# Kernel tuning notes

Hardware: AMD Instinct MI355X
Metric: run time of the kernel (lower is better)

## Reference

```python
import jax, jax.numpy as jnp
import numpy as np

D_MODEL = 768
NHEAD = 12
D_K = D_MODEL // NHEAD


def setup_inputs() -> dict:
    key = jax.random.key(0)
    ks = jax.random.split(key, 9)
    s = 1.0 / np.sqrt(D_MODEL)
    x = jax.random.normal(ks[0], (2, 4096, D_MODEL), dtype=jnp.float32)
    Wq = jax.random.uniform(ks[1], (D_MODEL, D_MODEL), jnp.float32, -s, s)
    bq = jax.random.uniform(ks[2], (D_MODEL,), jnp.float32, -s, s)
    Wk = jax.random.uniform(ks[3], (D_MODEL, D_MODEL), jnp.float32, -s, s)
    bk = jax.random.uniform(ks[4], (D_MODEL,), jnp.float32, -s, s)
    Wv = jax.random.uniform(ks[5], (D_MODEL, D_MODEL), jnp.float32, -s, s)
    bv = jax.random.uniform(ks[6], (D_MODEL,), jnp.float32, -s, s)
    Wo = jax.random.uniform(ks[7], (D_MODEL, D_MODEL), jnp.float32, -s, s)
    bo = jax.random.uniform(ks[8], (D_MODEL,), jnp.float32, -s, s)
    return {"x": x, "Wq": Wq, "bq": bq, "Wk": Wk, "bk": bk,
            "Wv": Wv, "bv": bv, "Wo": Wo, "bo": bo}


def reference(x, Wq, bq, Wk, bk, Wv, bv, Wo, bo):
    B, S, _ = x.shape
    # Linear layers: torch nn.Linear(y) = y @ W.T + b; weights stored [out,in]
    def split_heads(y):  # [B,S,D] -> [B,H,S,dk]
        return y.reshape(B, S, NHEAD, D_K).transpose(0, 2, 1, 3)
    Q = split_heads(x @ Wq.T + bq)
    K = split_heads(x @ Wk.T + bk)
    V = split_heads(x @ Wv.T + bv)
    scores = jnp.einsum('bhqd,bhkd->bhqk', Q, K) / jnp.sqrt(jnp.float32(D_K))
    attn = jax.nn.softmax(scores, axis=-1)
    context = jnp.einsum('bhqk,bhkd->bhqd', attn, V)
    context = context.transpose(0, 2, 1, 3).reshape(B, S, D_MODEL)
    return context @ Wo.T + bo
```

## Files before the change

kernel.cpp:

```cpp
#include <hip/hip_runtime.h>
#include <hip/hip_bf16.h>
#include <cstdint>

typedef __bf16 bf16;
typedef bf16 bf16x8 __attribute__((ext_vector_type(8)));
typedef float f32x4 __attribute__((ext_vector_type(4)));

#define MFMA16(a, b, c) __builtin_amdgcn_mfma_f32_16x16x32_bf16((a), (b), (c), 0, 0, 0)

constexpr int D_MODEL = 768;
constexpr int NHEAD = 12;
constexpr int DK = 64;
constexpr int SEQ = 4096;
constexpr int BATCH = 2;
constexpr int MROWS = BATCH * SEQ;
constexpr float QSCALE = 0.125f * 1.44269504089f;

__global__ void cvt_f32_to_bf16(const float* __restrict__ in, bf16* __restrict__ out, int n) {
    int i = (blockIdx.x * blockDim.x + threadIdx.x) * 4;
    if (i + 3 < n) {
        const float4 v = *reinterpret_cast<const float4*>(in + i);
        bf16 o0 = (bf16)v.x, o1 = (bf16)v.y, o2 = (bf16)v.z, o3 = (bf16)v.w;
        bf16 o[4] = {o0, o1, o2, o3};
        *reinterpret_cast<uint64_t*>(out + i) = *reinterpret_cast<uint64_t*>(o);
    }
}

__global__ __launch_bounds__(256, 2) void gemm_qkv(const bf16* __restrict__ A,
                                                   const float* __restrict__ Wq,
                                                   const float* __restrict__ Wk,
                                                   const float* __restrict__ Wv,
                                                   const float* __restrict__ bq,
                                                   const float* __restrict__ bk,
                                                   const float* __restrict__ bv,
                                                   bf16* __restrict__ Qb,
                                                   bf16* __restrict__ Kb,
                                                   bf16* __restrict__ Vtb) {
    constexpr int LDP = 88;
    __shared__ bf16 Asm[128][LDP];
    __shared__ bf16 Bsm[64][LDP];
    const int tid = threadIdx.x, lane = tid & 63, wid = tid >> 6;
    const int wm = wid >> 1, wn = wid & 1;
    const int m0 = blockIdx.x * 128;
    const int sel = blockIdx.y / 12;
    const int n0 = (blockIdx.y % 12) * 64;
    const float* Bw = sel == 0 ? Wq : (sel == 1 ? Wk : Wv);
    const float* bias = sel == 0 ? bq : (sel == 1 ? bk : bv);

    f32x4 acc[4][2];
#pragma unroll
    for (int i = 0; i < 4; i++)
#pragma unroll
        for (int j = 0; j < 2; j++) acc[i][j] = f32x4{0.f, 0.f, 0.f, 0.f};

    const int rr = tid >> 3, cc = (tid & 7) * 8;
    for (int k0 = 0; k0 < 768; k0 += 64) {
#pragma unroll
        for (int p = 0; p < 4; p++)
            *reinterpret_cast<bf16x8*>(&Asm[p * 32 + rr][cc]) =
                *reinterpret_cast<const bf16x8*>(A + (size_t)(m0 + p * 32 + rr) * 768 + k0 + cc);
#pragma unroll
        for (int p = 0; p < 2; p++) {
            const float* src = Bw + (size_t)(n0 + p * 32 + rr) * 768 + k0 + cc;
            const float4 f0 = *reinterpret_cast<const float4*>(src);
            const float4 f1 = *reinterpret_cast<const float4*>(src + 4);
            bf16x8 b8;
            b8[0] = (bf16)f0.x; b8[1] = (bf16)f0.y; b8[2] = (bf16)f0.z; b8[3] = (bf16)f0.w;
            b8[4] = (bf16)f1.x; b8[5] = (bf16)f1.y; b8[6] = (bf16)f1.z; b8[7] = (bf16)f1.w;
            *reinterpret_cast<bf16x8*>(&Bsm[p * 32 + rr][cc]) = b8;
        }
        __syncthreads();
#pragma unroll
        for (int kk = 0; kk < 64; kk += 32) {
            const int krd = kk + ((lane >> 4) << 3);
            bf16x8 af[4], bfr[2];
#pragma unroll
            for (int i = 0; i < 4; i++)
                af[i] = *reinterpret_cast<const bf16x8*>(&Asm[wm * 64 + i * 16 + (lane & 15)][krd]);
#pragma unroll
            for (int j = 0; j < 2; j++)
                bfr[j] = *reinterpret_cast<const bf16x8*>(&Bsm[wn * 32 + j * 16 + (lane & 15)][krd]);
#pragma unroll
            for (int i = 0; i < 4; i++)
#pragma unroll
                for (int j = 0; j < 2; j++) acc[i][j] = MFMA16(af[i], bfr[j], acc[i][j]);
        }
        __syncthreads();
    }

    const float scale = (sel == 0) ? QSCALE : 1.0f;
    const int rbase = m0 + wm * 64 + ((lane >> 4) << 2);
    const int cbase = n0 + wn * 32 + (lane & 15);
    bf16* obf = sel == 0 ? Qb : (sel == 1 ? Kb : Vtb);
#pragma unroll
    for (int i = 0; i < 4; i++) {
#pragma unroll
        for (int j = 0; j < 2; j++) {
            const int ncol = cbase + j * 16;
            const float bv = bias[ncol];
            const int h = ncol >> 6, d = ncol & 63;
#pragma unroll
            for (int r = 0; r < 4; r++) {
                const int mrow = rbase + i * 16 + r;
                const float v = (acc[i][j][r] + bv) * scale;
                const int b = mrow >> 12, s = mrow & 4095;
                if (sel < 2) {
                    obf[(((size_t)(b * NHEAD + h)) * SEQ + s) * DK + d] = (bf16)v;
                } else {
                    const int sp = (s & ~63) | (((s & 15) << 2) | ((s >> 4) & 3));
                    obf[(((size_t)(b * NHEAD + h)) * DK + d) * SEQ + sp] = (bf16)v;
                }
            }
        }
    }
}

__global__ __launch_bounds__(256, 2) void gemm_out(const bf16* __restrict__ A,
                                                   const float* __restrict__ Bw,
                                                   const float* __restrict__ bias,
                                                   float* __restrict__ ofl) {
    constexpr int LDP = 88;
    __shared__ bf16 Asm[128][LDP];
    __shared__ bf16 Bsm[64][LDP];
    const int tid = threadIdx.x, lane = tid & 63, wid = tid >> 6;
    const int wm = wid >> 1, wn = wid & 1;
    const int m0 = blockIdx.x * 128, n0 = blockIdx.y * 64;

    f32x4 acc[4][2];
#pragma unroll
    for (int i = 0; i < 4; i++)
#pragma unroll
        for (int j = 0; j < 2; j++) acc[i][j] = f32x4{0.f, 0.f, 0.f, 0.f};

    const int rr = tid >> 3, cc = (tid & 7) * 8;
    for (int k0 = 0; k0 < 768; k0 += 64) {
#pragma unroll
        for (int p = 0; p < 4; p++)
            *reinterpret_cast<bf16x8*>(&Asm[p * 32 + rr][cc]) =
                *reinterpret_cast<const bf16x8*>(A + (size_t)(m0 + p * 32 + rr) * 768 + k0 + cc);
#pragma unroll
        for (int p = 0; p < 2; p++) {
            const float* src = Bw + (size_t)(n0 + p * 32 + rr) * 768 + k0 + cc;
            const float4 f0 = *reinterpret_cast<const float4*>(src);
            const float4 f1 = *reinterpret_cast<const float4*>(src + 4);
            bf16x8 b8;
            b8[0] = (bf16)f0.x; b8[1] = (bf16)f0.y; b8[2] = (bf16)f0.z; b8[3] = (bf16)f0.w;
            b8[4] = (bf16)f1.x; b8[5] = (bf16)f1.y; b8[6] = (bf16)f1.z; b8[7] = (bf16)f1.w;
            *reinterpret_cast<bf16x8*>(&Bsm[p * 32 + rr][cc]) = b8;
        }
        __syncthreads();
#pragma unroll
        for (int kk = 0; kk < 64; kk += 32) {
            const int krd = kk + ((lane >> 4) << 3);
            bf16x8 af[4], bfr[2];
#pragma unroll
            for (int i = 0; i < 4; i++)
                af[i] = *reinterpret_cast<const bf16x8*>(&Asm[wm * 64 + i * 16 + (lane & 15)][krd]);
#pragma unroll
            for (int j = 0; j < 2; j++)
                bfr[j] = *reinterpret_cast<const bf16x8*>(&Bsm[wn * 32 + j * 16 + (lane & 15)][krd]);
#pragma unroll
            for (int i = 0; i < 4; i++)
#pragma unroll
                for (int j = 0; j < 2; j++) acc[i][j] = MFMA16(af[i], bfr[j], acc[i][j]);
        }
        __syncthreads();
    }

    const int rbase = m0 + wm * 64 + ((lane >> 4) << 2);
    const int cbase = n0 + wn * 32 + (lane & 15);
#pragma unroll
    for (int i = 0; i < 4; i++) {
#pragma unroll
        for (int j = 0; j < 2; j++) {
            const int ncol = cbase + j * 16;
            const float bv = bias[ncol];
#pragma unroll
            for (int r = 0; r < 4; r++) {
                const int mrow = rbase + i * 16 + r;
                ofl[(size_t)mrow * 768 + ncol] = acc[i][j][r] + bv;
            }
        }
    }
}

__global__ __launch_bounds__(256, 3) void attn_kernel(const bf16* __restrict__ Qb,
                                                      const bf16* __restrict__ Kb,
                                                      const bf16* __restrict__ Vtb,
                                                      bf16* __restrict__ ctx) {
    __shared__ bf16 Ksm[64][72];
    __shared__ bf16 Vts[64][72];
    __shared__ bf16 Psm[4][32][72];
    const int tid = threadIdx.x, l = tid & 63, w = tid >> 6;
    const int bh = blockIdx.y;
    const int q0 = blockIdx.x * 128;
    const bf16* Qh = Qb + (size_t)bh * SEQ * DK;
    const bf16* Kh = Kb + (size_t)bh * SEQ * DK;
    const bf16* Vth = Vtb + (size_t)bh * DK * SEQ;

    const int rsel = l & 15, csel = l >> 4;

    bf16x8 qf[2][2];
#pragma unroll
    for (int qi = 0; qi < 2; qi++) {
        const int qr = q0 + w * 32 + qi * 16 + rsel;
#pragma unroll
        for (int kk = 0; kk < 2; kk++)
            qf[qi][kk] = *reinterpret_cast<const bf16x8*>(Qh + (size_t)qr * DK + kk * 32 + csel * 8);
    }

    bf16x8 vones;
    {
        const bf16 ov = (rsel == 0) ? (bf16)1.0f : (bf16)0.0f;
#pragma unroll
        for (int j = 0; j < 8; j++) vones[j] = ov;
    }

    float m[2] = {-1e30f, -1e30f};
    f32x4 aco[2][4], aco_x[2];
#pragma unroll
    for (int qi = 0; qi < 2; qi++) {
#pragma unroll
        for (int f = 0; f < 4; f++) aco[qi][f] = f32x4{0.f, 0.f, 0.f, 0.f};
        aco_x[qi] = f32x4{0.f, 0.f, 0.f, 0.f};
    }

    const int srow = tid >> 2, sc4 = (tid & 3) * 16;

    bf16x8 pk0 = *reinterpret_cast<const bf16x8*>(Kh + (size_t)srow * DK + sc4);
    bf16x8 pk1 = *reinterpret_cast<const bf16x8*>(Kh + (size_t)srow * DK + sc4 + 8);
    bf16x8 pv0 = *reinterpret_cast<const bf16x8*>(Vth + (size_t)srow * SEQ + sc4);
    bf16x8 pv1 = *reinterpret_cast<const bf16x8*>(Vth + (size_t)srow * SEQ + sc4 + 8);

    constexpr int NT = SEQ / 64;
    for (int t = 0; t < NT; ++t) {
        __syncthreads();
        *reinterpret_cast<bf16x8*>(&Ksm[srow][sc4]) = pk0;
        *reinterpret_cast<bf16x8*>(&Ksm[srow][sc4 + 8]) = pk1;
        *reinterpret_cast<bf16x8*>(&Vts[srow][sc4]) = pv0;
        *reinterpret_cast<bf16x8*>(&Vts[srow][sc4 + 8]) = pv1;
        __syncthreads();

        if (t + 1 < NT) {
            const int kn = (t + 1) * 64;
            pk0 = *reinterpret_cast<const bf16x8*>(Kh + (size_t)(kn + srow) * DK + sc4);
            pk1 = *reinterpret_cast<const bf16x8*>(Kh + (size_t)(kn + srow) * DK + sc4 + 8);
            pv0 = *reinterpret_cast<const bf16x8*>(Vth + (size_t)srow * SEQ + kn + sc4);
            pv1 = *reinterpret_cast<const bf16x8*>(Vth + (size_t)srow * SEQ + kn + sc4 + 8);
        }

        f32x4 s4[2][4];
#pragma unroll
        for (int qi = 0; qi < 2; qi++)
#pragma unroll
            for (int f = 0; f < 4; f++) s4[qi][f] = f32x4{0.f, 0.f, 0.f, 0.f};
#pragma unroll
        for (int kk = 0; kk < 2; kk++) {
            const int krd = kk * 32 + csel * 8;
#pragma unroll
            for (int f = 0; f < 4; f++) {
                const bf16x8 kf = *reinterpret_cast<const bf16x8*>(&Ksm[f * 16 + rsel][krd]);
                s4[0][f] = MFMA16(qf[0][kk], kf, s4[0][f]);
                s4[1][f] = MFMA16(qf[1][kk], kf, s4[1][f]);
            }
        }

#pragma unroll
        for (int qi = 0; qi < 2; qi++) {
            float tm = s4[qi][0][0];
#pragma unroll
            for (int f = 0; f < 4; f++)
#pragma unroll
                for (int r = 0; r < 4; r++) tm = fmaxf(tm, s4[qi][f][r]);
            tm = fmaxf(tm, __shfl_xor(tm, 1));
            tm = fmaxf(tm, __shfl_xor(tm, 2));
            tm = fmaxf(tm, __shfl_xor(tm, 4));
            tm = fmaxf(tm, __shfl_xor(tm, 8));
            tm = fmaxf(tm, __shfl_xor(tm, 16));
            tm = fmaxf(tm, __shfl_xor(tm, 32));

            if (tm - m[qi] > 8.f) {
                const float scl = __builtin_amdgcn_exp2f(m[qi] - tm);
                m[qi] = tm;
#pragma unroll
                for (int f = 0; f < 4; f++)
#pragma unroll
                    for (int r = 0; r < 4; r++) aco[qi][f][r] *= scl;
#pragma unroll
                for (int r = 0; r < 4; r++) aco_x[qi][r] *= scl;
            }

#pragma unroll
            for (int r = 0; r < 4; r++) {
                union { bf16 h[4]; uint64_t u; } pk4;
#pragma unroll
                for (int f = 0; f < 4; f++)
                    pk4.h[f] = (bf16)__builtin_amdgcn_exp2f(s4[qi][f][r] - m[qi]);
                *reinterpret_cast<uint64_t*>(&Psm[w][qi * 16 + csel * 4 + r][rsel * 4]) = pk4.u;
            }
        }

#pragma unroll
        for (int ph = 0; ph < 2; ph++) {
            const int kc = ph * 32 + csel * 8;
            const bf16x8 pf0 = *reinterpret_cast<const bf16x8*>(&Psm[w][rsel][kc]);
            const bf16x8 pf1 = *reinterpret_cast<const bf16x8*>(&Psm[w][16 + rsel][kc]);
#pragma unroll
            for (int f2 = 0; f2 < 4; f2++) {
                const bf16x8 vf = *reinterpret_cast<const bf16x8*>(&Vts[f2 * 16 + rsel][kc]);
                aco[0][f2] = MFMA16(pf0, vf, aco[0][f2]);
                aco[1][f2] = MFMA16(pf1, vf, aco[1][f2]);
            }
            aco_x[0] = MFMA16(pf0, vones, aco_x[0]);
            aco_x[1] = MFMA16(pf1, vones, aco_x[1]);
        }
    }

    const int b = bh / NHEAD, h = bh % NHEAD;
#pragma unroll
    for (int qi = 0; qi < 2; qi++) {
        float inv[4];
#pragma unroll
        for (int r = 0; r < 4; r++) inv[r] = 1.0f / __shfl(aco_x[qi][r], l & 48);
#pragma unroll
        for (int f = 0; f < 4; f++)
#pragma unroll
            for (int r = 0; r < 4; r++) {
                const int q = q0 + w * 32 + qi * 16 + csel * 4 + r;
                const int d = f * 16 + rsel;
                ctx[((size_t)b * SEQ + q) * D_MODEL + h * DK + d] = (bf16)(aco[qi][f][r] * inv[r]);
            }
    }
}

extern "C" void kernel_launch(void* const* d_in, const int* in_sizes, int n_in,
                              void* d_out, int out_size, void* d_ws, size_t ws_size,
                              hipStream_t stream) {
    const float* x  = (const float*)d_in[0];
    const float* Wq = (const float*)d_in[1];
    const float* bq = (const float*)d_in[2];
    const float* Wk = (const float*)d_in[3];
    const float* bk = (const float*)d_in[4];
    const float* Wv = (const float*)d_in[5];
    const float* bv = (const float*)d_in[6];
    const float* Wo = (const float*)d_in[7];
    const float* bo = (const float*)d_in[8];
    float* out = (float*)d_out;

    char* ws = (char*)d_ws;
    size_t off = 0;
    auto alloc = [&](size_t bytes) { void* p = ws + off; off += (bytes + 255) & ~(size_t)255; return p; };
    bf16* xb   = (bf16*)alloc((size_t)MROWS * 768 * 2);
    bf16* Qb   = (bf16*)alloc((size_t)BATCH * NHEAD * SEQ * DK * 2);
    bf16* Kb   = (bf16*)alloc((size_t)BATCH * NHEAD * SEQ * DK * 2);
    bf16* Vtb  = (bf16*)alloc((size_t)BATCH * NHEAD * SEQ * DK * 2);
    bf16* ctxb = (bf16*)alloc((size_t)MROWS * 768 * 2);

    const int nx = MROWS * 768;
    cvt_f32_to_bf16<<<nx / (256 * 4), 256, 0, stream>>>(x, xb, nx);

    gemm_qkv<<<dim3(MROWS / 128, 36), 256, 0, stream>>>(xb, Wq, Wk, Wv, bq, bk, bv, Qb, Kb, Vtb);

    attn_kernel<<<dim3(SEQ / 128, BATCH * NHEAD), 256, 0, stream>>>(Qb, Kb, Vtb, ctxb);

    gemm_out<<<dim3(MROWS / 128, 768 / 64), 256, 0, stream>>>(ctxb, Wo, bo, out);
}
```

Before: 235.4 us.

## Fuse x bf16 conversion into QKV GEMM and share softmax max across wave

Drops the separate fp32-to-bf16 conversion kernel for x. The QKV GEMM now loads fp32 x directly and converts it while staging into shared memory, which removes one launch and a round trip of the bf16 copy through memory. The cost is that each x tile is re-read as fp32 by all 36 column blocks, doubling those load bytes. In attention, the two per-query-group running maxima are merged into a single wave-wide maximum, and the cross-lane shuffle reduction and rescale run only when some lane's max grows past the threshold. This skips most shuffles but risks more bf16 underflow for rows whose scores sit well below the shared max.

```diff
diff --git a/kernel.cpp b/kernel.cpp
--- a/kernel.cpp
+++ b/kernel.cpp
@@ -16,17 +16,7 @@
 constexpr int MROWS = BATCH * SEQ;
 constexpr float QSCALE = 0.125f * 1.44269504089f;
 
-__global__ void cvt_f32_to_bf16(const float* __restrict__ in, bf16* __restrict__ out, int n) {
-    int i = (blockIdx.x * blockDim.x + threadIdx.x) * 4;
-    if (i + 3 < n) {
-        const float4 v = *reinterpret_cast<const float4*>(in + i);
-        bf16 o0 = (bf16)v.x, o1 = (bf16)v.y, o2 = (bf16)v.z, o3 = (bf16)v.w;
-        bf16 o[4] = {o0, o1, o2, o3};
-        *reinterpret_cast<uint64_t*>(out + i) = *reinterpret_cast<uint64_t*>(o);
-    }
-}
-
-__global__ __launch_bounds__(256, 2) void gemm_qkv(const bf16* __restrict__ A,
+__global__ __launch_bounds__(256, 2) void gemm_qkv(const float* __restrict__ X,
                                                    const float* __restrict__ Wq,
                                                    const float* __restrict__ Wk,
                                                    const float* __restrict__ Wv,
@@ -56,9 +46,15 @@
     const int rr = tid >> 3, cc = (tid & 7) * 8;
     for (int k0 = 0; k0 < 768; k0 += 64) {
 #pragma unroll
-        for (int p = 0; p < 4; p++)
-            *reinterpret_cast<bf16x8*>(&Asm[p * 32 + rr][cc]) =
-                *reinterpret_cast<const bf16x8*>(A + (size_t)(m0 + p * 32 + rr) * 768 + k0 + cc);
+        for (int p = 0; p < 4; p++) {
+            const float* src = X + (size_t)(m0 + p * 32 + rr) * 768 + k0 + cc;
+            const float4 f0 = *reinterpret_cast<const float4*>(src);
+            const float4 f1 = *reinterpret_cast<const float4*>(src + 4);
+            bf16x8 a8;
+            a8[0] = (bf16)f0.x; a8[1] = (bf16)f0.y; a8[2] = (bf16)f0.z; a8[3] = (bf16)f0.w;
+            a8[4] = (bf16)f1.x; a8[5] = (bf16)f1.y; a8[6] = (bf16)f1.z; a8[7] = (bf16)f1.w;
+            *reinterpret_cast<bf16x8*>(&Asm[p * 32 + rr][cc]) = a8;
+        }
 #pragma unroll
         for (int p = 0; p < 2; p++) {
             const float* src = Bw + (size_t)(n0 + p * 32 + rr) * 768 + k0 + cc;
@@ -216,7 +212,7 @@
         for (int j = 0; j < 8; j++) vones[j] = ov;
     }
 
-    float m[2] = {-1e30f, -1e30f};
+    float m = -1e30f;
     f32x4 aco[2][4], aco_x[2];
 #pragma unroll
     for (int qi = 0; qi < 2; qi++) {
@@ -265,23 +261,24 @@
             }
         }
 
-#pragma unroll
-        for (int qi = 0; qi < 2; qi++) {
-            float tm = s4[qi][0][0];
+        float tm = s4[0][0][0];
+#pragma unroll
+        for (int qi = 0; qi < 2; qi++)
 #pragma unroll
             for (int f = 0; f < 4; f++)
 #pragma unroll
                 for (int r = 0; r < 4; r++) tm = fmaxf(tm, s4[qi][f][r]);
+        if (__any(tm - m > 8.f)) {
             tm = fmaxf(tm, __shfl_xor(tm, 1));
             tm = fmaxf(tm, __shfl_xor(tm, 2));
             tm = fmaxf(tm, __shfl_xor(tm, 4));
             tm = fmaxf(tm, __shfl_xor(tm, 8));
             tm = fmaxf(tm, __shfl_xor(tm, 16));
             tm = fmaxf(tm, __shfl_xor(tm, 32));
-
-            if (tm - m[qi] > 8.f) {
-                const float scl = __builtin_amdgcn_exp2f(m[qi] - tm);
-                m[qi] = tm;
+            const float scl = __builtin_amdgcn_exp2f(m - tm);
+            m = tm;
+#pragma unroll
+            for (int qi = 0; qi < 2; qi++) {
 #pragma unroll
                 for (int f = 0; f < 4; f++)
 #pragma unroll
@@ -289,16 +286,18 @@
 #pragma unroll
                 for (int r = 0; r < 4; r++) aco_x[qi][r] *= scl;
             }
-
+        }
+
+#pragma unroll
+        for (int qi = 0; qi < 2; qi++)
 #pragma unroll
             for (int r = 0; r < 4; r++) {
                 union { bf16 h[4]; uint64_t u; } pk4;
 #pragma unroll
                 for (int f = 0; f < 4; f++)
-                    pk4.h[f] = (bf16)__builtin_amdgcn_exp2f(s4[qi][f][r] - m[qi]);
+                    pk4.h[f] = (bf16)__builtin_amdgcn_exp2f(s4[qi][f][r] - m);
                 *reinterpret_cast<uint64_t*>(&Psm[w][qi * 16 + csel * 4 + r][rsel * 4]) = pk4.u;
             }
-        }
 
 #pragma unroll
         for (int ph = 0; ph < 2; ph++) {
@@ -350,16 +349,12 @@
     char* ws = (char*)d_ws;
     size_t off = 0;
     auto alloc = [&](size_t bytes) { void* p = ws + off; off += (bytes + 255) & ~(size_t)255; return p; };
-    bf16* xb   = (bf16*)alloc((size_t)MROWS * 768 * 2);
     bf16* Qb   = (bf16*)alloc((size_t)BATCH * NHEAD * SEQ * DK * 2);
     bf16* Kb   = (bf16*)alloc((size_t)BATCH * NHEAD * SEQ * DK * 2);
     bf16* Vtb  = (bf16*)alloc((size_t)BATCH * NHEAD * SEQ * DK * 2);
     bf16* ctxb = (bf16*)alloc((size_t)MROWS * 768 * 2);
 
-    const int nx = MROWS * 768;
-    cvt_f32_to_bf16<<<nx / (256 * 4), 256, 0, stream>>>(x, xb, nx);
-
-    gemm_qkv<<<dim3(MROWS / 128, 36), 256, 0, stream>>>(xb, Wq, Wk, Wv, bq, bk, bv, Qb, Kb, Vtb);
+    gemm_qkv<<<dim3(MROWS / 128, 36), 256, 0, stream>>>(x, Wq, Wk, Wv, bq, bk, bv, Qb, Kb, Vtb);
 
     attn_kernel<<<dim3(SEQ / 128, BATCH * NHEAD), 256, 0, stream>>>(Qb, Kb, Vtb, ctxb);
 
```

After: 222.1 us. -5.7%, faster.
